# Optimization experiments

Measured on AMD Instinct MI355X. Metric: run time of the kernel, lower is better.

The kernel has to match this reference:

```python
import jax, jax.numpy as jnp
import numpy as np

HEADS = 4


def setup_inputs() -> dict:
    key = jax.random.key(0)
    ks = jax.random.split(key, 6)
    b, c, d, h, w = 4, 512, 16, 16, 16
    x = jax.random.normal(ks[0], (b, c, d, h, w), dtype=jnp.float32)
    s = 0.02  # param init scale
    Wq = jax.random.normal(ks[1], (c, c), dtype=jnp.float32) * s
    Wk = jax.random.normal(ks[2], (c, c), dtype=jnp.float32) * s
    Wv = jax.random.normal(ks[3], (c, c), dtype=jnp.float32) * s
    Wproj = jax.random.normal(ks[4], (c, c), dtype=jnp.float32) * s
    bproj = jnp.zeros((c,), dtype=jnp.float32)
    return {"x": x, "Wq": Wq, "Wk": Wk, "Wv": Wv, "Wproj": Wproj, "bproj": bproj}


def reference(x, Wq, Wk, Wv, Wproj, bproj):
    b, c, d, h, w = x.shape
    N = d * h * w
    scale = (c // HEADS) ** -0.5  # module uses ch//heads for scale
    xf = x.reshape(b, c, N)  # (b, c, N)
    # 1x1 Conv1d == channel matmul
    q = jnp.einsum('oc,bcn->bon', Wq, xf)
    k = jnp.einsum('oc,bcn->bon', Wk, xf)
    v = jnp.einsum('oc,bcn->bon', Wv, xf)
    # Faithful to original (buggy) view: split SEQUENCE dim by heads -> (b, H, c, N//H)
    q = q.reshape(b, HEADS, c, N // HEADS)
    k = k.reshape(b, HEADS, c, N // HEADS)
    v = v.reshape(b, HEADS, c, N // HEADS)
    attn = jax.nn.softmax(jnp.einsum('bhqe,bhke->bhqk', q, k) * scale, axis=-1)
    out = jnp.einsum('bhqk,bhke->bhqe', attn, v)  # (b, H, c, N//H)
    out = jnp.swapaxes(out, 2, 3).reshape(b, c, N)  # matches transpose(2,3).view
    out = jnp.einsum('oc,bcn->bon', Wproj, out) + bproj[None, :, None]
    return out.reshape(b, c, d, h, w) + x
```

## Files before the change

### kernel.cpp

```cpp
#include <hip/hip_runtime.h>
#include <stdint.h>


typedef __attribute__((ext_vector_type(8))) short short8;
typedef __attribute__((ext_vector_type(4))) float f32x4;

typedef const __attribute__((address_space(1))) unsigned int* gas_ptr;
typedef __attribute__((address_space(3))) unsigned int* las_ptr;

#define ATTN_SCALE 0.08838834764831845f

__device__ __forceinline__ unsigned short f2bf(float f) {
    union { float f; unsigned int u; } c; c.f = f;
    unsigned int u = c.u;
    u += 0x7fffu + ((u >> 16) & 1u);
    return (unsigned short)(u >> 16);
}

__device__ __forceinline__ void gl_lds16(const void* g, void* l) {
    __builtin_amdgcn_global_load_lds((gas_ptr)(uintptr_t)g, (las_ptr)(uintptr_t)l,
                                     16, 0, 0);
}

template<int LDA, int LDB, int KDIM, bool PERMB = false>
__device__ __forceinline__ void mfma_core(
    const unsigned short* __restrict__ A,
    const unsigned short* __restrict__ B,
    int m0, int n0,
    unsigned short* __restrict__ sA, unsigned short* __restrict__ sB,
    f32x4 acc[4][4])
{
    const int tid  = threadIdx.x;
    const int lane = tid & 63, wave = tid >> 6;
    const int lr = lane >> 2, lc = lane & 3;
    const int lcs = lc ^ ((lr >> 1) & 3);
    const int wm = (wave & 1) * 64, wn = (wave >> 1) * 64;
    const int col = lane & 15, quad = lane >> 4;
    const int swz = (quad ^ ((col >> 1) & 3)) * 8;

    const unsigned short* ga = A + (size_t)(m0 + 32 * wave + lr) * LDA + lcs * 8;
    int rb0 = n0 + 32 * wave + lr;
    int rb1 = rb0 + 16;
    if (PERMB) {
        rb0 = 4 * (rb0 & 127) + (rb0 >> 7);
        rb1 = 4 * (rb1 & 127) + (rb1 >> 7);
    }
    const unsigned short* gb0 = B + (size_t)rb0 * LDB + lcs * 8;
    const unsigned short* gb1 = B + (size_t)rb1 * LDB + lcs * 8;

    const int wr0 = (32 * wave) * 32;
    const int wr1 = (32 * wave + 16) * 32;

    gl_lds16(ga,            sA + wr0);
    gl_lds16(ga + 16 * LDA, sA + wr1);
    gl_lds16(gb0,           sB + wr0);
    gl_lds16(gb1,           sB + wr1);

    constexpr int NK = KDIM / 32;
    for (int kk = 0; kk < NK; ++kk) {
        const int bo = (kk & 1) * 4096;
        if (kk + 1 < NK) {
            const int nb = ((kk + 1) & 1) * 4096;
            const int k0 = (kk + 1) * 32;
            gl_lds16(ga + k0,            sA + nb + wr0);
            gl_lds16(ga + k0 + 16 * LDA, sA + nb + wr1);
            gl_lds16(gb0 + k0,           sB + nb + wr0);
            gl_lds16(gb1 + k0,           sB + nb + wr1);
            asm volatile("s_waitcnt vmcnt(4)" ::: "memory");
        } else {
            asm volatile("s_waitcnt vmcnt(0)" ::: "memory");
        }
        __builtin_amdgcn_s_barrier();
        asm volatile("" ::: "memory");
        __builtin_amdgcn_sched_barrier(0);

        const unsigned short* bA = sA + bo;
        const unsigned short* bB = sB + bo;
        short8 af[4], bfv[4];
        #pragma unroll
        for (int i = 0; i < 4; ++i)
            af[i] = *(const short8*)&bA[(wm + i * 16 + col) * 32 + swz];
        #pragma unroll
        for (int j = 0; j < 4; ++j)
            bfv[j] = *(const short8*)&bB[(wn + j * 16 + col) * 32 + swz];
        #pragma unroll
        for (int i = 0; i < 4; ++i)
            #pragma unroll
            for (int j = 0; j < 4; ++j)
                acc[i][j] = __builtin_amdgcn_mfma_f32_16x16x32_bf16(
                    af[i], bfv[j], acc[i][j], 0, 0, 0);

        __builtin_amdgcn_s_barrier();
        asm volatile("" ::: "memory");
    }
}

__global__ __launch_bounds__(256)
void prep(const float* __restrict__ x,
          const float* __restrict__ Wq, const float* __restrict__ Wk,
          const float* __restrict__ Wv, const float* __restrict__ Wp,
          unsigned short* __restrict__ xT, unsigned short* __restrict__ Wb)
{
    if (blockIdx.z == 4) {
        const int idx = (blockIdx.y * 64 + blockIdx.x) * 256 + threadIdx.x;
        const int mat = idx >> 16;
        const int off = (idx & 65535) << 2;
        const float* src = (mat == 0 ? Wq : mat == 1 ? Wk : mat == 2 ? Wv : Wp) + off;
        const float4 f = *(const float4*)src;
        uint2 o;
        o.x = f2bf(f.x) | ((unsigned)f2bf(f.y) << 16);
        o.y = f2bf(f.z) | ((unsigned)f2bf(f.w) << 16);
        *(uint2*)&Wb[mat * 262144 + off] = o;
        return;
    }
    const int b = blockIdx.z;
    const int l = threadIdx.x & 63, w = threadIdx.x >> 6;
    const int n  = blockIdx.x * 64 + l;
    const int c0 = blockIdx.y * 32 + w * 8;
    const float* xp = x + (size_t)b * 2097152 + (size_t)c0 * 4096 + n;
    unsigned int p[4];
    #pragma unroll
    for (int j = 0; j < 4; ++j) {
        const unsigned short a  = f2bf(xp[(2 * j)     * 4096]);
        const unsigned short bb = f2bf(xp[(2 * j + 1) * 4096]);
        p[j] = a | ((unsigned)bb << 16);
    }
    uint4 v; v.x = p[0]; v.y = p[1]; v.z = p[2]; v.w = p[3];
    *(uint4*)&xT[(size_t)b * 2097152 + (size_t)n * 512 + c0] = v;
}

__global__ __launch_bounds__(256)
void gemm_qkv(const unsigned short* __restrict__ Wb,
              const unsigned short* __restrict__ xT,
              unsigned short* __restrict__ qb, unsigned short* __restrict__ kb,
              unsigned short* __restrict__ vT)
{
    __shared__ unsigned short sT[128 * 136];
    unsigned short* sA = sT;
    unsigned short* sB = sT + 8192;

    const int d = blockIdx.x + 32 * blockIdx.y + 128 * blockIdx.z;
    const int f = (d & 7) * 192 + (d >> 3);
    const int g = f >> 7, q = f & 127;
    const int wsel = g % 3, b = g / 3;
    const int m0 = (q & 3) * 128, n0 = (q >> 2) * 128;

    const unsigned short* A = Wb + wsel * 262144;
    const unsigned short* B = xT + (size_t)b * 2097152;

    f32x4 z4 = {0.f, 0.f, 0.f, 0.f};
    f32x4 acc[4][4];
    #pragma unroll
    for (int i = 0; i < 4; ++i)
        #pragma unroll
        for (int j = 0; j < 4; ++j) acc[i][j] = z4;

    mfma_core<512, 512, 512>(A, B, m0, n0, sA, sB, acc);

    __syncthreads();

    const int tid = threadIdx.x;
    const int lane = tid & 63, wave = tid >> 6;
    const int wm = (wave & 1) * 64, wn = (wave >> 1) * 64;
    const int col = lane & 15, quad = lane >> 4;
    const int h = m0 >> 7, s = n0 >> 10;

    if (wsel < 2) {
        #pragma unroll
        for (int i = 0; i < 4; ++i)
            #pragma unroll
            for (int r = 0; r < 4; ++r) {
                const int rr = wm + i * 16 + quad * 4 + r;
                #pragma unroll
                for (int j = 0; j < 4; ++j)
                    sT[rr * 136 + wn + j * 16 + col] = f2bf(acc[i][j][r]);
            }
        __syncthreads();
        unsigned short* C = (wsel == 0 ? qb : kb)
                          + (size_t)(b * 4 + h) * 524288;
        const int bKc = (n0 & 1023) >> 5;
        const int u = tid & 15, v = (tid >> 4) & 3, wv = tid >> 6;
        unsigned short* dst = C + (size_t)(s * 256 + bKc + wv) * 512
                            + (v * 16 + u) * 8;
        const unsigned short* src = sT + u * 136 + wv * 32 + v * 8;
        #pragma unroll
        for (int k = 0; k < 8; ++k)
            *(uint4*)(dst + k * 16384) = *(const uint4*)(src + k * 2176);
    } else {
        #pragma unroll
        for (int i = 0; i < 4; ++i)
            #pragma unroll
            for (int r = 0; r < 4; ++r) {
                const int rr = wm + i * 16 + quad * 4 + r;
                #pragma unroll
                for (int j = 0; j < 4; ++j)
                    sT[(wn + j * 16 + col) * 136 + rr] = f2bf(acc[i][j][r]);
            }
        __syncthreads();
        const int e0 = n0 & 1023;
        unsigned short* dst = vT + (size_t)(b * 4 + h) * 524288 + s * 128;
        const int u = tid & 15, rsel = tid >> 4;
        #pragma unroll
        for (int k = 0; k < 8; ++k) {
            const int ee = rsel + k * 16;
            *(uint4*)&dst[(size_t)(e0 + ee) * 512 + u * 8] =
                *(const uint4*)&sT[ee * 136 + u * 8];
        }
    }
}

__global__ __launch_bounds__(1024)
void gemm_qks(const unsigned short* __restrict__ qb,
              const unsigned short* __restrict__ kb,
              unsigned short* __restrict__ P)
{
    __shared__ float red[2][32][8];
    const int d = blockIdx.x;
    const int flat = (d & 7) * 32 + (d >> 3);
    const int rg = flat & 15, z = flat >> 4;
    const unsigned short* Aq = qb + (size_t)z * 524288;
    const unsigned short* Bk = kb + (size_t)z * 524288;
    unsigned short* Pz = P + (size_t)z * 262144;

    const int tid = threadIdx.x;
    const int lane = tid & 63, w = tid >> 6;
    const int rw = w >> 3, cw = w & 7;
    const int col = lane & 15, quad = lane >> 4;

    const unsigned short* ap  = Aq + (size_t)((rg * 2 + rw) * 32) * 512 + lane * 8;
    const unsigned short* bp0 = Bk + (size_t)((cw * 4 + 0) * 32) * 512 + lane * 8;
    const unsigned short* bp1 = bp0 + 16384;
    const unsigned short* bp2 = bp0 + 32768;
    const unsigned short* bp3 = bp0 + 49152;

    f32x4 z4 = {0.f, 0.f, 0.f, 0.f};
    f32x4 acc[4];
    #pragma unroll
    for (int g = 0; g < 4; ++g) acc[g] = z4;

    #pragma unroll 4
    for (int kk = 0; kk < 32; ++kk) {
        const int o = kk * 512;
        const short8 af = *(const short8*)(ap + o);
        short8 bf[4];
        bf[0] = *(const short8*)(bp0 + o);
        bf[1] = *(const short8*)(bp1 + o);
        bf[2] = *(const short8*)(bp2 + o);
        bf[3] = *(const short8*)(bp3 + o);
        #pragma unroll
        for (int g = 0; g < 4; ++g)
            acc[g] = __builtin_amdgcn_mfma_f32_16x16x32_bf16(
                af, bf[g], acc[g], 0, 0, 0);
    }

    float mx[4];
    #pragma unroll
    for (int r = 0; r < 4; ++r) {
        float m = acc[0][r];
        #pragma unroll
        for (int g = 1; g < 4; ++g) m = fmaxf(m, acc[g][r]);
        #pragma unroll
        for (int s = 1; s < 16; s <<= 1) m = fmaxf(m, __shfl_xor(m, s));
        mx[r] = m;
    }
    if (col == 0) {
        #pragma unroll
        for (int r = 0; r < 4; ++r)
            red[0][rw * 16 + quad * 4 + r][cw] = mx[r];
    }
    __syncthreads();
    float sm[4];
    #pragma unroll
    for (int r = 0; r < 4; ++r) {
        const int row = rw * 16 + quad * 4 + r;
        float m = red[0][row][0];
        #pragma unroll
        for (int t = 1; t < 8; ++t) m = fmaxf(m, red[0][row][t]);
        float s = 0.f;
        #pragma unroll
        for (int g = 0; g < 4; ++g) {
            const float e = __expf((acc[g][r] - m) * ATTN_SCALE);
            acc[g][r] = e;
            s += e;
        }
        #pragma unroll
        for (int t = 1; t < 16; t <<= 1) s += __shfl_xor(s, t);
        sm[r] = s;
    }
    if (col == 0) {
        #pragma unroll
        for (int r = 0; r < 4; ++r)
            red[1][rw * 16 + quad * 4 + r][cw] = sm[r];
    }
    __syncthreads();
    #pragma unroll
    for (int r = 0; r < 4; ++r) {
        const int row = rw * 16 + quad * 4 + r;
        float tot = red[1][row][0];
        #pragma unroll
        for (int t = 1; t < 8; ++t) tot += red[1][row][t];
        const float inv = 1.f / tot;
        unsigned short* op = Pz + (size_t)(rg * 32 + row) * 512 + cw * 64 + col;
        #pragma unroll
        for (int g = 0; g < 4; ++g)
            op[g * 16] = f2bf(acc[g][r] * inv);
    }
}

__global__ __launch_bounds__(256)
void gemm_pv(const unsigned short* __restrict__ Pb,
             const unsigned short* __restrict__ vT,
             unsigned short* __restrict__ yT)
{
    __shared__ unsigned short sT[128 * 136];
    unsigned short* sA = sT;
    unsigned short* sB = sT + 8192;

    const int d = blockIdx.x + 8 * blockIdx.y + 32 * blockIdx.z;
    const int f = (d & 7) * 64 + (d >> 3);
    const int n0 = (f & 7) * 128;
    const int m0 = ((f >> 3) & 3) * 128;
    const int z = f >> 5, b = z >> 2, hh = z & 3;

    const unsigned short* A = Pb + (size_t)z * 262144;
    const unsigned short* B = vT + (size_t)z * 524288;
    unsigned short* yTb = yT + (size_t)b * 2097152;

    f32x4 z4 = {0.f, 0.f, 0.f, 0.f};
    f32x4 acc[4][4];
    #pragma unroll
    for (int i = 0; i < 4; ++i)
        #pragma unroll
        for (int j = 0; j < 4; ++j) acc[i][j] = z4;

    mfma_core<512, 512, 512>(A, B, m0, n0, sA, sB, acc);

    __syncthreads();

    const int tid = threadIdx.x;
    const int lane = tid & 63, wave = tid >> 6;
    const int wm = (wave & 1) * 64, wn = (wave >> 1) * 64;
    const int col = lane & 15, quad = lane >> 4;

    #pragma unroll
    for (int i = 0; i < 4; ++i)
        #pragma unroll
        for (int r = 0; r < 4; ++r) {
            const int rr = wm + i * 16 + quad * 4 + r;
            #pragma unroll
            for (int j = 0; j < 4; ++j)
                sT[rr * 136 + wn + j * 16 + col] = f2bf(acc[i][j][r]);
        }
    __syncthreads();

    const int sblk = m0 >> 7;
    #pragma unroll
    for (int k = 0; k < 4; ++k) {
        const int rid = k * 256 + tid;
        const int qq_l = rid >> 3, s = rid & 7;
        const unsigned short* Trow = sT + qq_l * 136;
        unsigned int p[8];
        #pragma unroll
        for (int t = 0; t < 8; ++t) {
            const unsigned int a  = Trow[s + 8 * (2 * t)];
            const unsigned int bb = Trow[s + 8 * (2 * t + 1)];
            p[t] = a | (bb << 16);
        }
        const size_t base = (size_t)((s << 9) + 4 * qq_l + sblk) * 512
                          + hh * 128 + (n0 >> 3);
        uint4 lo; lo.x = p[0]; lo.y = p[1]; lo.z = p[2]; lo.w = p[3];
        uint4 hi; hi.x = p[4]; hi.y = p[5]; hi.z = p[6]; hi.w = p[7];
        *(uint4*)&yTb[base]     = lo;
        *(uint4*)&yTb[base + 8] = hi;
    }
}

__global__ __launch_bounds__(256)
void gemm_proj(const unsigned short* __restrict__ Wpb,
               const unsigned short* __restrict__ yT,
               const float* __restrict__ bias, const float* __restrict__ x,
               float* __restrict__ out)
{
    __shared__ unsigned short sA[2 * 128 * 32], sB[2 * 128 * 32];

    const int d = blockIdx.x + 32 * blockIdx.y + 128 * blockIdx.z;
    const int f = (d & 7) * 64 + (d >> 3);
    const int n0 = (f & 31) * 128;
    const int m0 = ((f >> 5) & 3) * 128;
    const int b  = f >> 7;

    const unsigned short* B = yT + (size_t)b * 2097152;

    f32x4 z4 = {0.f, 0.f, 0.f, 0.f};
    f32x4 acc[4][4];
    #pragma unroll
    for (int i = 0; i < 4; ++i)
        #pragma unroll
        for (int j = 0; j < 4; ++j) acc[i][j] = z4;

    mfma_core<512, 512, 512>(Wpb, B, m0, n0, sA, sB, acc);

    const int lane = threadIdx.x & 63, wave = threadIdx.x >> 6;
    const int wm = (wave & 1) * 64, wn = (wave >> 1) * 64;
    const int col = lane & 15, quad = lane >> 4;
    const size_t boff = (size_t)b * 2097152;
    #pragma unroll
    for (int i = 0; i < 4; ++i)
        #pragma unroll
        for (int r = 0; r < 4; ++r) {
            const int row = m0 + wm + i * 16 + quad * 4 + r;
            const float bi = bias[row];
            #pragma unroll
            for (int j = 0; j < 4; ++j) {
                const size_t idx = boff + (size_t)row * 4096 + n0 + wn + j * 16 + col;
                out[idx] = acc[i][j][r] + bi + x[idx];
            }
        }
}

extern "C" void kernel_launch(void* const* d_in, const int* in_sizes, int n_in,
                              void* d_out, int out_size, void* d_ws, size_t ws_size,
                              hipStream_t stream) {
    const float* x     = (const float*)d_in[0];
    const float* Wq    = (const float*)d_in[1];
    const float* Wk    = (const float*)d_in[2];
    const float* Wv    = (const float*)d_in[3];
    const float* Wproj = (const float*)d_in[4];
    const float* bproj = (const float*)d_in[5];
    float* out = (float*)d_out;

    char* w = (char*)d_ws;
    unsigned short* xT = (unsigned short*)(w + 0);
    unsigned short* qb = (unsigned short*)(w + 16777216);
    unsigned short* kb = (unsigned short*)(w + 33554432);
    unsigned short* vT = (unsigned short*)(w + 50331648);
    unsigned short* Pb = (unsigned short*)(w + 100663296);
    unsigned short* Wb = (unsigned short*)(w + 109051904);
    unsigned short* yT = xT;

    prep        <<<dim3(64, 16, 5),  256, 0, stream>>>(x, Wq, Wk, Wv, Wproj, xT, Wb);
    gemm_qkv    <<<dim3(32, 4, 12),  256, 0, stream>>>(Wb, xT, qb, kb, vT);
    gemm_qks    <<<dim3(256),        1024, 0, stream>>>(qb, kb, Pb);
    gemm_pv     <<<dim3(8, 4, 16),   256, 0, stream>>>(Pb, vT, yT);
    gemm_proj   <<<dim3(32, 4, 4),   256, 0, stream>>>(Wb + 3 * 262144, yT, bproj, x, out);
}
```

Measured before the change: 202.4 us.

## Drop XCD-aware block swizzles and halve softmax block size in gemm_qks

Removes the block-index remapping (the d&7-based swizzles) in gemm_qkv, gemm_pv and gemm_proj, so blocks use plain blockIdx-derived tile coordinates. gemm_qks now uses 512-thread blocks covering 16 query rows instead of 1024 threads covering 32, and launches twice as many blocks. The smaller blocks aim for better occupancy and a lower barrier cost in the softmax kernel. In exchange, each k tile is reread by more blocks, and dropping the swizzle may hurt L2 locality across XCDs.

```diff
diff --git a/kernel.cpp b/kernel.cpp
--- a/kernel.cpp
+++ b/kernel.cpp
@@ -139,14 +139,10 @@
     unsigned short* sA = sT;
     unsigned short* sB = sT + 8192;
 
-    const int d = blockIdx.x + 32 * blockIdx.y + 128 * blockIdx.z;
-    const int f = (d & 7) * 192 + (d >> 3);
-    const int g = f >> 7, q = f & 127;
-    const int wsel = g % 3, b = g / 3;
-    const int m0 = (q & 3) * 128, n0 = (q >> 2) * 128;
-
+    const int z = blockIdx.z, wsel = z >> 2, b = z & 3;
     const unsigned short* A = Wb + wsel * 262144;
     const unsigned short* B = xT + (size_t)b * 2097152;
+    const int m0 = blockIdx.y * 128, n0 = blockIdx.x * 128;
 
     f32x4 z4 = {0.f, 0.f, 0.f, 0.f};
     f32x4 acc[4][4];
@@ -209,25 +205,24 @@
     }
 }
 
-__global__ __launch_bounds__(1024)
+__global__ __launch_bounds__(512)
 void gemm_qks(const unsigned short* __restrict__ qb,
               const unsigned short* __restrict__ kb,
               unsigned short* __restrict__ P)
 {
-    __shared__ float red[2][32][8];
+    __shared__ float red[2][16][8];
     const int d = blockIdx.x;
-    const int flat = (d & 7) * 32 + (d >> 3);
-    const int rg = flat & 15, z = flat >> 4;
+    const int f = (d & 7) * 64 + (d >> 3);
+    const int rg = f & 31, z = f >> 5;
     const unsigned short* Aq = qb + (size_t)z * 524288;
     const unsigned short* Bk = kb + (size_t)z * 524288;
     unsigned short* Pz = P + (size_t)z * 262144;
 
     const int tid = threadIdx.x;
-    const int lane = tid & 63, w = tid >> 6;
-    const int rw = w >> 3, cw = w & 7;
+    const int lane = tid & 63, cw = tid >> 6;
     const int col = lane & 15, quad = lane >> 4;
 
-    const unsigned short* ap  = Aq + (size_t)((rg * 2 + rw) * 32) * 512 + lane * 8;
+    const unsigned short* ap  = Aq + (size_t)(rg * 32) * 512 + lane * 8;
     const unsigned short* bp0 = Bk + (size_t)((cw * 4 + 0) * 32) * 512 + lane * 8;
     const unsigned short* bp1 = bp0 + 16384;
     const unsigned short* bp2 = bp0 + 32768;
@@ -266,13 +261,13 @@
     if (col == 0) {
         #pragma unroll
         for (int r = 0; r < 4; ++r)
-            red[0][rw * 16 + quad * 4 + r][cw] = mx[r];
+            red[0][quad * 4 + r][cw] = mx[r];
     }
     __syncthreads();
     float sm[4];
     #pragma unroll
     for (int r = 0; r < 4; ++r) {
-        const int row = rw * 16 + quad * 4 + r;
+        const int row = quad * 4 + r;
         float m = red[0][row][0];
         #pragma unroll
         for (int t = 1; t < 8; ++t) m = fmaxf(m, red[0][row][t]);
@@ -290,17 +285,17 @@
     if (col == 0) {
         #pragma unroll
         for (int r = 0; r < 4; ++r)
-            red[1][rw * 16 + quad * 4 + r][cw] = sm[r];
+            red[1][quad * 4 + r][cw] = sm[r];
     }
     __syncthreads();
     #pragma unroll
     for (int r = 0; r < 4; ++r) {
-        const int row = rw * 16 + quad * 4 + r;
+        const int row = quad * 4 + r;
         float tot = red[1][row][0];
         #pragma unroll
         for (int t = 1; t < 8; ++t) tot += red[1][row][t];
         const float inv = 1.f / tot;
-        unsigned short* op = Pz + (size_t)(rg * 32 + row) * 512 + cw * 64 + col;
+        unsigned short* op = Pz + (size_t)(rg * 16 + row) * 512 + cw * 64 + col;
         #pragma unroll
         for (int g = 0; g < 4; ++g)
             op[g * 16] = f2bf(acc[g][r] * inv);
@@ -315,16 +310,12 @@
     __shared__ unsigned short sT[128 * 136];
     unsigned short* sA = sT;
     unsigned short* sB = sT + 8192;
-
-    const int d = blockIdx.x + 8 * blockIdx.y + 32 * blockIdx.z;
-    const int f = (d & 7) * 64 + (d >> 3);
-    const int n0 = (f & 7) * 128;
-    const int m0 = ((f >> 3) & 3) * 128;
-    const int z = f >> 5, b = z >> 2, hh = z & 3;
-
+    const int z = blockIdx.z, b = z >> 2, hh = z & 3;
     const unsigned short* A = Pb + (size_t)z * 262144;
     const unsigned short* B = vT + (size_t)z * 524288;
     unsigned short* yTb = yT + (size_t)b * 2097152;
+    const int m0 = blockIdx.y * 128;
+    const int n0 = blockIdx.x * 128;
 
     f32x4 z4 = {0.f, 0.f, 0.f, 0.f};
     f32x4 acc[4][4];
@@ -382,14 +373,9 @@
                float* __restrict__ out)
 {
     __shared__ unsigned short sA[2 * 128 * 32], sB[2 * 128 * 32];
-
-    const int d = blockIdx.x + 32 * blockIdx.y + 128 * blockIdx.z;
-    const int f = (d & 7) * 64 + (d >> 3);
-    const int n0 = (f & 31) * 128;
-    const int m0 = ((f >> 5) & 3) * 128;
-    const int b  = f >> 7;
-
+    const int b = blockIdx.z;
     const unsigned short* B = yT + (size_t)b * 2097152;
+    const int m0 = blockIdx.y * 128, n0 = blockIdx.x * 128;
 
     f32x4 z4 = {0.f, 0.f, 0.f, 0.f};
     f32x4 acc[4][4];
@@ -440,7 +426,7 @@
 
     prep        <<<dim3(64, 16, 5),  256, 0, stream>>>(x, Wq, Wk, Wv, Wproj, xT, Wb);
     gemm_qkv    <<<dim3(32, 4, 12),  256, 0, stream>>>(Wb, xT, qb, kb, vT);
-    gemm_qks    <<<dim3(256),        1024, 0, stream>>>(qb, kb, Pb);
+    gemm_qks    <<<dim3(512),        512, 0, stream>>>(qb, kb, Pb);
     gemm_pv     <<<dim3(8, 4, 16),   256, 0, stream>>>(Pb, vT, yT);
     gemm_proj   <<<dim3(32, 4, 4),   256, 0, stream>>>(Wb + 3 * 262144, yT, bproj, x, out);
 }
```

Measured after the change: 205.3 us. Within noise of the previous version (+1.5%).
